# Performance work log

Hardware: AMD Instinct MI355X
Metric: run time of the kernel (lower is better)

Reference implementation:

```python
import jax, jax.numpy as jnp
import numpy as np

T, B = 1024, 128
IDIM, CDIM, N, M = 256, 512, 128, 64


def setup_inputs() -> dict:
    key = jax.random.key(0)
    ks = jax.random.split(key, 10)
    stdev = 5.0 / np.sqrt(IDIM + M + CDIM)  # matches _reset_controller
    u = lambda k, shp: jax.random.uniform(k, shp, jnp.float32, -stdev, stdev)
    return {
        "embs": jax.random.normal(ks[0], (T, B, IDIM), jnp.float32),
        "ilen": T // 2,
        # LSTM controller params (PyTorch layout: [4*cdim, in] / [4*cdim, cdim])
        "w_ih": u(ks[1], (4 * CDIM, IDIM + M)),
        "w_hh": u(ks[2], (4 * CDIM, CDIM)),
        "b_ih": jnp.zeros((4 * CDIM,), jnp.float32),
        "b_hh": jnp.zeros((4 * CDIM,), jnp.float32),
        "h0": jax.random.normal(ks[3], (CDIM,), jnp.float32) * 0.05,
        "c0": jax.random.normal(ks[4], (CDIM,), jnp.float32) * 0.05,
        "r0": jax.random.normal(ks[5], (1, M), jnp.float32) * 0.02,
        # memory head params (concrete subclass): write address / write value / read address
        "W_wa": jax.random.normal(ks[6], (N, CDIM), jnp.float32) * 0.02,
        "b_wa": jnp.zeros((N,), jnp.float32),
        "W_wv": jax.random.normal(ks[7], (M, IDIM), jnp.float32) * 0.02,
        "b_wv": jnp.zeros((M,), jnp.float32),
        "W_ra": jax.random.normal(ks[8], (N, CDIM), jnp.float32) * 0.02,
        "b_ra": jnp.zeros((N,), jnp.float32),
    }


def _forward(embs, w_ih, w_hh, b_ih, b_hh, h0, c0, r0,
             W_wa, b_wa, W_wv, b_wv, W_ra, b_ra, ilen):
    bsz = embs.shape[1]
    h = jnp.broadcast_to(h0, (bsz, CDIM))
    c = jnp.broadcast_to(c0, (bsz, CDIM))
    r = jnp.broadcast_to(r0, (bsz, M))
    mem = jnp.zeros((bsz, N, M), embs.dtype)
    b = b_ih + b_hh

    def step(carry, xt):
        h, c, r, mem = carry
        emb, t = xt  # emb: [B, idim]
        x = jnp.concatenate([emb, r], axis=-1)            # [B, idim+M]
        gates = x @ w_ih.T + h @ w_hh.T + b               # [B, 4*cdim]
        i, f, g, o = jnp.split(gates, 4, axis=-1)         # torch gate order i,f,g,o
        c_new = jax.nn.sigmoid(f) * c + jax.nn.sigmoid(i) * jnp.tanh(g)
        h_new = jax.nn.sigmoid(o) * jnp.tanh(c_new)       # controller_outp
        is_write = t < ilen
        # write(controller_outp, emb): additive write at softmax address
        wa = jax.nn.softmax(h_new @ W_wa.T + b_wa, axis=-1)   # [B, N]
        v = emb @ W_wv.T + b_wv                               # [B, M]
        mem_new = jnp.where(is_write, mem + wa[:, :, None] * v[:, None, :], mem)
        # read(controller_outp): softmax-addressed weighted sum over slots
        ra = jax.nn.softmax(h_new @ W_ra.T + b_ra, axis=-1)   # [B, N]
        r_read = jnp.einsum('bn,bnm->bm', ra, mem_new)        # [B, M]
        r_new = jnp.where(is_write, r, r_read)
        out = jnp.concatenate([h_new, r_new], axis=-1)        # [B, cdim+M]
        return (h_new, c_new, r_new, mem_new), out

    _, os = jax.lax.scan(step, (h, c, r, mem),
                         (embs, jnp.arange(embs.shape[0])))
    return os  # [T, B, cdim+M]


def reference(embs, ilen, w_ih, w_hh, b_ih, b_hh, h0, c0, r0,
              W_wa, b_wa, W_wv, b_wv, W_ra, b_ra):
    return _forward(embs, w_ih, w_hh, b_ih, b_hh, h0, c0, r0,
                    W_wa, b_wa, W_wv, b_wv, W_ra, b_ra, ilen)
```

## Files before the change

### kernel.cpp

```cpp
#include <hip/hip_runtime.h>

typedef _Float16 f16;
typedef __attribute__((ext_vector_type(8))) _Float16 half8;
typedef __attribute__((ext_vector_type(2))) _Float16 half2v;
typedef __attribute__((ext_vector_type(4))) float f32x4;
typedef __attribute__((ext_vector_type(4))) unsigned int u32x4;
typedef unsigned long long u64;

#define TSTEPS 1024

static const size_t OFF_WP   = 0;
static const size_t OFF_WVP  = 3407872;
static const size_t OFF_BIAS = 3440640;
static const size_t OFF_EMBP = 3448832;
static const size_t OFF_V    = 70557696;
static const size_t OFF_XH   = 87334912;
static const size_t OFF_XR   = 87597056;
static const size_t OFF_FLG  = 87629824;
static const size_t OFF_MEM  = 87630848;
static const size_t WS_NEED  = 91825152;


__global__ void marnn_packw(const float* __restrict__ w_ih, const float* __restrict__ w_hh,
                            const float* __restrict__ b_ih, const float* __restrict__ b_hh,
                            f16* __restrict__ WP, float* __restrict__ biasP) {
  int idx = blockIdx.x * 256 + threadIdx.x;
  if (idx < 2048) {
    int j = idx >> 2, g = idx & 3, rg = g * 512 + j;
    biasP[idx] = b_ih[rg] + b_hh[rg];
  }
  if (idx >= 1703936) return;
  int e = idx & 7, l = (idx >> 3) & 63;
  int q = idx >> 9;
  int ks = q % 26; int ntile = q / 26;
  int n = ntile * 16 + (l & 15);
  int k = ks * 32 + (l >> 4) * 8 + e;
  int j2 = n >> 2, g2 = n & 3, rg2 = g2 * 512 + j2;
  float v = (k < 320) ? w_ih[(size_t)rg2 * 320 + k] : w_hh[(size_t)rg2 * 512 + (k - 320)];
  WP[idx] = (f16)v;
}

__global__ void marnn_packwv(const float* __restrict__ W_wv, f16* __restrict__ WVP) {
  int idx = blockIdx.x * 256 + threadIdx.x;
  if (idx >= 16384) return;
  int e = idx & 7, l = (idx >> 3) & 63, ks = (idx >> 9) & 7, nt = idx >> 12;
  int n = nt * 16 + (l & 15);
  int k = ks * 32 + (l >> 4) * 8 + e;
  WVP[idx] = (f16)W_wv[n * 256 + k];
}

__global__ void marnn_packemb(const float* __restrict__ embs, f16* __restrict__ embsP) {
  const long total8 = (long)1024 * 128 * 32;
  const long stride = (long)gridDim.x * blockDim.x;
  for (long i8 = (long)blockIdx.x * blockDim.x + threadIdx.x; i8 < total8; i8 += stride) {
    int bl = (int)(i8 & 15), kc = (int)((i8 >> 4) & 31), bg = (int)((i8 >> 9) & 7);
    long t = i8 >> 12;
    const float* s = embs + ((t * 128) + bg * 16 + bl) * 256 + kc * 8;
    f32x4 a = *(const f32x4*)s, b = *(const f32x4*)(s + 4);
    half8 h;
    h[0]=(f16)a[0]; h[1]=(f16)a[1]; h[2]=(f16)a[2]; h[3]=(f16)a[3];
    h[4]=(f16)b[0]; h[5]=(f16)b[1]; h[6]=(f16)b[2]; h[7]=(f16)b[3];
    *(half8*)(embsP + i8 * 8) = h;
  }
}

__global__ __launch_bounds__(256)
void marnn_vpre(const f16* __restrict__ embsP, const f16* __restrict__ WVP,
                const float* __restrict__ b_wv, f16* __restrict__ Vh) {
  const int tb = blockIdx.x;
  const int wv = threadIdx.x >> 6, l = threadIdx.x & 63;
  half8 bf[8];
  #pragma unroll
  for (int ks = 0; ks < 8; ++ks)
    bf[ks] = *(const half8*)(WVP + ((size_t)(wv * 8 + ks) * 64 + l) * 8);
  const f16* ab = embsP + (size_t)tb * 4096;
  f32x4 acc = {0.f, 0.f, 0.f, 0.f};
  #pragma unroll
  for (int ks = 0; ks < 8; ++ks) {
    half8 af = *(const half8*)(ab + ((size_t)(ks * 4 + (l >> 4)) * 16 + (l & 15)) * 8);
    acc = __builtin_amdgcn_mfma_f32_16x16x32_f16(bf[ks], af, acc, 0, 0, 0);
  }
  const int b = (tb & 7) * 16 + (l & 15);
  const long t = tb >> 3;
  #pragma unroll
  for (int r = 0; r < 4; ++r) {
    int m = wv * 16 + (l >> 4) * 4 + r;
    Vh[((t * 128) + b) * 64 + m] = (f16)(acc[r] + b_wv[m]);
  }
}


struct __align__(16) MarnnSMem {
  f16  whead[128 * 512];
  char xl[26624];
  char un[4096];
};

__device__ __forceinline__ float marnn_dot8(half8 a, half8 b, float acc) {
#if __has_builtin(__builtin_amdgcn_fdot2)
  half2v a0 = {a[0],a[1]}, a1 = {a[2],a[3]}, a2 = {a[4],a[5]}, a3 = {a[6],a[7]};
  half2v b0 = {b[0],b[1]}, b1 = {b[2],b[3]}, b2 = {b[4],b[5]}, b3 = {b[6],b[7]};
  acc = __builtin_amdgcn_fdot2(a0, b0, acc, false);
  acc = __builtin_amdgcn_fdot2(a1, b1, acc, false);
  acc = __builtin_amdgcn_fdot2(a2, b2, acc, false);
  acc = __builtin_amdgcn_fdot2(a3, b3, acc, false);
#else
  #pragma unroll
  for (int e = 0; e < 8; ++e) acc += (float)a[e] * (float)b[e];
#endif
  return acc;
}

__device__ __forceinline__ float fast_sigmoid(float x) {
  return __builtin_amdgcn_rcpf(1.f + __expf(-x));
}
__device__ __forceinline__ float fast_tanh(float x) {
  return 1.f - 2.f * __builtin_amdgcn_rcpf(1.f + __expf(2.f * x));
}

__device__ __forceinline__ unsigned ld_flag(const unsigned* p) {
  return __hip_atomic_load(p, __ATOMIC_RELAXED, __HIP_MEMORY_SCOPE_AGENT);
}
__device__ __forceinline__ void st_flag(unsigned* p, unsigned v) {
  __hip_atomic_store(p, v, __ATOMIC_RELAXED, __HIP_MEMORY_SCOPE_AGENT);
}
__device__ __forceinline__ u64 ld_llc64(const void* p) {
  return __hip_atomic_load((const u64*)p, __ATOMIC_RELAXED, __HIP_MEMORY_SCOPE_AGENT);
}
__device__ __forceinline__ void st_llc32(void* p, unsigned v) {
  __hip_atomic_store((unsigned*)p, v, __ATOMIC_RELAXED, __HIP_MEMORY_SCOPE_AGENT);
}

__device__ __forceinline__ void poll16(const unsigned* line, unsigned ep) {
  int l = threadIdx.x & 63;
  for (;;) {
    unsigned v = (l < 16) ? ld_flag(line + l) : ep;
    if (__all((int)(v >= ep))) break;
    __builtin_amdgcn_s_sleep(1);
  }
  asm volatile("" ::: "memory");
}

__global__ __launch_bounds__(512, 1)
void marnn_main(const int* __restrict__ ilen_p, const float* __restrict__ h0,
                const float* __restrict__ c0, const float* __restrict__ r0,
                const float* __restrict__ W_wa, const float* __restrict__ b_wa,
                const float* __restrict__ W_ra, const float* __restrict__ b_ra,
                float* __restrict__ out, char* __restrict__ ws) {
  __shared__ MarnnSMem sm;

  const f16*   WP    = (const f16*)(ws + OFF_WP);
  const float* biasP = (const float*)(ws + OFF_BIAS);
  const f16*   embsP = (const f16*)(ws + OFF_EMBP);
  const f16*   Vh    = (const f16*)(ws + OFF_V);
  unsigned*    XH    = (unsigned*)(ws + OFF_XH);
  unsigned*    XR    = (unsigned*)(ws + OFF_XR);
  unsigned*    FLG   = (unsigned*)(ws + OFF_FLG);
  float*       MEMB  = (float*)(ws + OFF_MEM);

  const int blk = blockIdx.x, tid = threadIdx.x;
  const int wav = tid >> 6, lane = tid & 63;
  const int g = blk & 7, ns = blk >> 3;
  const int ilen = ilen_p[0];
  unsigned* gfh = FLG + g * 32;
  unsigned* gfr = gfh + 16;

  half8 bfr[26];
  {
    const f16* wpb = WP + ((size_t)(ns * 8 + wav) * 26) * 512 + lane * 8;
    #pragma unroll
    for (int ks = 0; ks < 26; ++ks) bfr[ks] = *(const half8*)(wpb + ks * 512);
  }

  auto loadWhead = [&](const float* Wsrc) {
    for (int i = tid; i < 8192; i += 512) {
      int n = i >> 6, slot = i & 63;
      const float* s = Wsrc + n * 512 + slot * 8;
      f32x4 a = *(const f32x4*)(s), b2 = *(const f32x4*)(s + 4);
      half8 hv;
      hv[0]=(f16)a[0]; hv[1]=(f16)a[1]; hv[2]=(f16)a[2]; hv[3]=(f16)a[3];
      hv[4]=(f16)b2[0]; hv[5]=(f16)b2[1]; hv[6]=(f16)b2[2]; hv[7]=(f16)b2[3];
      *(half8*)((char*)sm.whead + (n << 10) + (((slot + n) & 63) << 4)) = hv;
    }
  };
  loadWhead(ilen > 0 ? W_wa : W_ra);

  {
    const u32x4* s0 = (const u32x4*)(embsP + (size_t)g * 4096);
    ((u32x4*)sm.xl)[tid] = s0[tid];
    const float* hsrc0 = h0 + (tid >> 3) * 8;
    half8 hv;
    #pragma unroll
    for (int e = 0; e < 8; ++e) hv[e] = (f16)hsrc0[e];
    *(half8*)(sm.xl + 10240 + tid * 32) = hv;
    *(half8*)(sm.xl + 10240 + tid * 32 + 16) = hv;
  }
  __syncthreads();

  const int b_lane = lane & 15, sel = lane >> 4;
  const int jg = ns * 32 + wav * 4 + sel;
  float c = c0[jg];
  const f32x4 bias4 = *(const f32x4*)(biasP + jg * 4);
  const float r0v = (tid < 64) ? r0[tid] : 0.f;
  const int b = g * 16 + ns;

  const float bw0 = b_wa[lane], bw1 = b_wa[lane + 64];
  const float br0 = b_ra[lane], br1 = b_ra[lane + 64];
  const int gn = (wav & 3) * 32 + (lane & 31);
  const int kq = ((wav >> 2) << 1) | (lane >> 5);

  half8 rf0, rf1;
  #pragma unroll
  for (int e = 0; e < 8; ++e) {
    rf0[e] = (f16)r0[sel * 8 + e];
    rf1[e] = (f16)r0[32 + sel * 8 + e];
  }

  for (int t = 0; t < TSTEPS; ++t) {
    const int par = t & 1, nxt = par ^ 1;
    const bool iswrite = (t < ilen);

    u32x4 sa = {0u, 0u, 0u, 0u};
    if (t + 1 < TSTEPS)
      sa = ((const u32x4*)(embsP + (((size_t)(t + 1) * 8) + g) * 4096))[tid];
    half8 vh = {};
    if (iswrite && wav == 4 && lane < 8)
      vh = *(const half8*)(Vh + ((size_t)t * 128 + b) * 64 + lane * 8);

    if (t > ilen && wav == 0) {
      poll16(gfr, (unsigned)(t - ilen));
      const u64* rsrc = (const u64*)XR + ((size_t)par * 8 + g) * 256;
      #pragma unroll
      for (int i = 0; i < 4; ++i) {
        int v = i * 64 + lane;
        u64 d = ld_llc64(rsrc + v);
        int bb = v >> 4;
        int m0 = (v & 15) * 4;
        char* dst = sm.xl + 8192 + ((m0 >= 32) ? 1024 : 0)
                    + (((m0 & 31) >> 3) * 256) + bb * 16 + (m0 & 7) * 2;
        *(u64*)dst = d;
      }
    }
    f32x4 acc0 = {0.f, 0.f, 0.f, 0.f}, acc1 = {0.f, 0.f, 0.f, 0.f};
    const char* xb = sm.xl + sel * 256 + b_lane * 16;
    #pragma unroll
    for (int ks = 0; ks < 8; ++ks) {
      half8 af = *(const half8*)(xb + ks * 1024);
      if (ks & 1) acc1 = __builtin_amdgcn_mfma_f32_16x16x32_f16(bfr[ks], af, acc1, 0, 0, 0);
      else        acc0 = __builtin_amdgcn_mfma_f32_16x16x32_f16(bfr[ks], af, acc0, 0, 0, 0);
    }
    #pragma unroll
    for (int ks = 10; ks < 26; ++ks) {
      half8 af = *(const half8*)(xb + ks * 1024);
      if (ks & 1) acc1 = __builtin_amdgcn_mfma_f32_16x16x32_f16(bfr[ks], af, acc1, 0, 0, 0);
      else        acc0 = __builtin_amdgcn_mfma_f32_16x16x32_f16(bfr[ks], af, acc0, 0, 0, 0);
    }
    if (t <= ilen) {
      acc0 = __builtin_amdgcn_mfma_f32_16x16x32_f16(bfr[8], rf0, acc0, 0, 0, 0);
      acc1 = __builtin_amdgcn_mfma_f32_16x16x32_f16(bfr[9], rf1, acc1, 0, 0, 0);
    } else {
      __syncthreads();
      acc0 = __builtin_amdgcn_mfma_f32_16x16x32_f16(bfr[8], *(const half8*)(xb + 8 * 1024), acc0, 0, 0, 0);
      acc1 = __builtin_amdgcn_mfma_f32_16x16x32_f16(bfr[9], *(const half8*)(xb + 9 * 1024), acc1, 0, 0, 0);
    }
    const f32x4 acc = acc0 + acc1;

    float h;
    {
      float si = fast_sigmoid(acc[0] + bias4[0]);
      float sf = fast_sigmoid(acc[1] + bias4[1]);
      float so = fast_sigmoid(acc[3] + bias4[3]);
      c = sf * c + si * fast_tanh(acc[2] + bias4[2]);
      h = so * fast_tanh(c);
      union { f16 f; unsigned short u; } cv; cv.f = (f16)h;
      unsigned hu = cv.u;
      unsigned pu = __shfl_down(hu, 16, 64);
      if (!(sel & 1))
        st_llc32(XH + ((size_t)nxt * 8 + g) * 4096
                   + ns * 256 + wav * 32 + b_lane * 2 + (sel >> 1),
                 hu | (pu << 16));
    }
    asm volatile("s_waitcnt vmcnt(0)" ::: "memory");
    __syncthreads();
    if (tid == 0) st_flag(gfh + ns, (unsigned)(t + 1));
    __builtin_nontemporal_store(h, &out[(size_t)t * 73728 + (g * 16 + b_lane) * 576 + jg]);
    if (wav == 0) poll16(gfh, (unsigned)(t + 1));
    __syncthreads();

    {
      ((u32x4*)sm.xl)[tid] = sa;
      const u64* hsrc = (const u64*)XH + ((size_t)nxt * 8 + g) * 2048;
      #pragma unroll
      for (int i = 0; i < 4; ++i) {
        int v = i * 512 + tid;
        u64 d = ld_llc64(hsrc + v);
        int nsp = v >> 7;
        int wvp = (v >> 4) & 7;
        int bb = v & 15;
        int j0 = nsp * 32 + wvp * 4;
        char* dst = sm.xl + 10240 + ((j0 >> 3) * 256) + bb * 16 + (j0 & 7) * 2;
        *(u64*)dst = d;
      }
    }
    __syncthreads();

    if (t == ilen) { loadWhead(W_ra); __syncthreads(); }
    float* vpart = (float*)sm.un;
    float* vred  = (float*)(sm.un + 1024);
    float* vsec  = (float*)(sm.un + 3072);
    {
      if (iswrite && wav == 4 && lane < 8) {
        f32x4 lo = {(float)vh[0], (float)vh[1], (float)vh[2], (float)vh[3]};
        f32x4 hi = {(float)vh[4], (float)vh[5], (float)vh[6], (float)vh[7]};
        *(f32x4*)(vsec + lane * 8) = lo;
        *(f32x4*)(vsec + lane * 8 + 4) = hi;
      }
      const char* wrow = (const char*)sm.whead + (gn << 10);
      const char* hbase = sm.xl + 10240 + ns * 16;
      float av0 = 0.f, av1 = 0.f;
      #pragma unroll
      for (int i = 0; i < 16; i += 2) {
        int s0 = kq * 16 + i;
        av0 = marnn_dot8(*(const half8*)(wrow + (((s0 + gn) & 63) << 4)),
                         *(const half8*)(hbase + s0 * 256), av0);
        av1 = marnn_dot8(*(const half8*)(wrow + (((s0 + 1 + gn) & 63) << 4)),
                         *(const half8*)(hbase + (s0 + 1) * 256), av1);
      }
      float av = av0 + av1;
      av += __shfl_xor(av, 32, 64);
      if (lane < 32) vpart[((wav >> 2) << 7) + gn] = av;
    }
    __syncthreads();

    float p0, p1;
    {
      float l0 = vpart[lane] + vpart[128 + lane] + (iswrite ? bw0 : br0);
      float l1 = vpart[64 + lane] + vpart[192 + lane] + (iswrite ? bw1 : br1);
      float mx = fmaxf(l0, l1);
      #pragma unroll
      for (int off = 32; off > 0; off >>= 1) mx = fmaxf(mx, __shfl_xor(mx, off, 64));
      float e0 = __expf(l0 - mx), e1 = __expf(l1 - mx);
      float s = e0 + e1;
      #pragma unroll
      for (int off = 32; off > 0; off >>= 1) s += __shfl_xor(s, off, 64);
      float inv = __builtin_amdgcn_rcpf(s);
      p0 = e0 * inv; p1 = e1 * inv;
    }

    if (iswrite) {
      int n = tid >> 2;
      float pA = __shfl(p0, n & 63, 64);
      float pB = __shfl(p1, n & 63, 64);
      float p = (n < 64) ? pA : pB;
      float* mrow = MEMB + (((size_t)b) * 128 + n) * 64 + (tid & 3) * 16;
      const float* vv = vsec + (tid & 3) * 16;
      #pragma unroll
      for (int i2 = 0; i2 < 16; i2 += 4) {
        f32x4 mm = *(f32x4*)(mrow + i2);
        f32x4 v4 = *(const f32x4*)(vv + i2);
        mm = mm + p * v4;
        *(f32x4*)(mrow + i2) = mm;
      }
      if (tid < 64)
        __builtin_nontemporal_store(r0v, &out[(size_t)t * 73728 + b * 576 + 512 + tid]);
    } else {
      const int m = tid & 63;
      const float* mcol = MEMB + (((size_t)b) * 128 + wav * 16) * 64 + m;
      float a0 = 0.f, a1 = 0.f;
      #pragma unroll
      for (int n2 = 0; n2 < 16; n2 += 2) {
        float q0 = __shfl((wav < 4) ? p0 : p1, (wav * 16 + n2) & 63, 64);
        float q1 = __shfl((wav < 4) ? p0 : p1, (wav * 16 + n2 + 1) & 63, 64);
        a0 = fmaf(q0, mcol[n2 * 64], a0);
        a1 = fmaf(q1, mcol[(n2 + 1) * 64], a1);
      }
      vred[wav * 64 + m] = a0 + a1;
      __syncthreads();
      if (tid < 64) {
        float rv = 0.f;
        #pragma unroll
        for (int nc = 0; nc < 8; ++nc) rv += vred[nc * 64 + tid];
        union { f16 f; unsigned short u; } cr; cr.f = (f16)rv;
        unsigned ru = cr.u;
        unsigned rp = __shfl_down(ru, 1, 64);
        if (!(tid & 1))
          st_llc32(XR + ((size_t)nxt * 8 + g) * 512 + ns * 32 + (tid >> 1),
                   ru | (rp << 16));
        asm volatile("s_waitcnt vmcnt(0)" ::: "memory");
        if (tid == 0) st_flag(gfr + ns, (unsigned)(t - ilen + 1));
        __builtin_nontemporal_store(rv, &out[(size_t)t * 73728 + b * 576 + 512 + tid]);
      }
    }
  }
}


extern "C" void kernel_launch(void* const* d_in, const int* in_sizes, int n_in,
                              void* d_out, int out_size, void* d_ws, size_t ws_size,
                              hipStream_t stream) {
  const float* embs = (const float*)d_in[0];
  const int*   ilen = (const int*)d_in[1];
  const float* w_ih = (const float*)d_in[2];
  const float* w_hh = (const float*)d_in[3];
  const float* b_ih = (const float*)d_in[4];
  const float* b_hh = (const float*)d_in[5];
  const float* h0   = (const float*)d_in[6];
  const float* c0   = (const float*)d_in[7];
  const float* r0   = (const float*)d_in[8];
  const float* W_wa = (const float*)d_in[9];
  const float* b_wa = (const float*)d_in[10];
  const float* W_wv = (const float*)d_in[11];
  const float* b_wv = (const float*)d_in[12];
  const float* W_ra = (const float*)d_in[13];
  const float* b_ra = (const float*)d_in[14];
  float* out = (float*)d_out;
  char* ws = (char*)d_ws;
  if (ws_size < WS_NEED) return;

  hipMemsetAsync(ws + OFF_FLG, 0, 1024, stream);
  hipMemsetAsync(ws + OFF_MEM, 0, 4194304, stream);
  marnn_packw<<<6656, 256, 0, stream>>>(w_ih, w_hh, b_ih, b_hh,
                                        (f16*)(ws + OFF_WP), (float*)(ws + OFF_BIAS));
  marnn_packwv<<<64, 256, 0, stream>>>(W_wv, (f16*)(ws + OFF_WVP));
  marnn_packemb<<<2048, 256, 0, stream>>>(embs, (f16*)(ws + OFF_EMBP));
  marnn_vpre<<<8192, 256, 0, stream>>>((const f16*)(ws + OFF_EMBP), (const f16*)(ws + OFF_WVP),
                                       b_wv, (f16*)(ws + OFF_V));
  marnn_main<<<128, 512, 0, stream>>>(ilen, h0, c0, r0, W_wa, b_wa, W_ra, b_ra, out, ws);
}
```

Measured before the change: 6.163 ms.

## Distribute head-address projection across blocks via MFMA partial sums exchanged in L2

Each block no longer keeps the full 128x512 head weight in LDS and computes all address logits with dot products. Instead, each block computes a partial logit for its own 32-column slice of h with one MFMA from register-resident fragments. The partials are published through a global exchange buffer with an extra flag, and each block sums the 16 partials before the softmax. This removes the per-step full head matvec and the weight reload at the write/read switch. In exchange it adds two more block barriers and an extra cross-block exchange in fp16, which may cost precision. The fetch of the read vector is also moved inside the read-phase branch.

New measurement: 6.196 ms. No clear change (+0.5%).

```diff
diff --git a/kernel.cpp b/kernel.cpp
--- a/kernel.cpp
+++ b/kernel.cpp
@@ -2,7 +2,6 @@
 
 typedef _Float16 f16;
 typedef __attribute__((ext_vector_type(8))) _Float16 half8;
-typedef __attribute__((ext_vector_type(2))) _Float16 half2v;
 typedef __attribute__((ext_vector_type(4))) float f32x4;
 typedef __attribute__((ext_vector_type(4))) unsigned int u32x4;
 typedef unsigned long long u64;
@@ -16,9 +15,10 @@
 static const size_t OFF_V    = 70557696;
 static const size_t OFF_XH   = 87334912;
 static const size_t OFF_XR   = 87597056;
-static const size_t OFF_FLG  = 87629824;
-static const size_t OFF_MEM  = 87630848;
-static const size_t WS_NEED  = 91825152;
+static const size_t OFF_XP   = 87629824;
+static const size_t OFF_FLG  = 88678400;
+static const size_t OFF_MEM  = 88680448;
+static const size_t WS_NEED  = 92874752;
 
 
 __global__ void marnn_packw(const float* __restrict__ w_ih, const float* __restrict__ w_hh,
@@ -91,25 +91,13 @@
 
 
 struct __align__(16) MarnnSMem {
-  f16  whead[128 * 512];
-  char xl[26624];
-  char un[4096];
+  char  xl[26624];
+  f16   hlocal[512];
+  f16   plocal[2048];
+  float pacc[1024];
+  float vred[512];
+  float vsec[64];
 };
-
-__device__ __forceinline__ float marnn_dot8(half8 a, half8 b, float acc) {
-#if __has_builtin(__builtin_amdgcn_fdot2)
-  half2v a0 = {a[0],a[1]}, a1 = {a[2],a[3]}, a2 = {a[4],a[5]}, a3 = {a[6],a[7]};
-  half2v b0 = {b[0],b[1]}, b1 = {b[2],b[3]}, b2 = {b[4],b[5]}, b3 = {b[6],b[7]};
-  acc = __builtin_amdgcn_fdot2(a0, b0, acc, false);
-  acc = __builtin_amdgcn_fdot2(a1, b1, acc, false);
-  acc = __builtin_amdgcn_fdot2(a2, b2, acc, false);
-  acc = __builtin_amdgcn_fdot2(a3, b3, acc, false);
-#else
-  #pragma unroll
-  for (int e = 0; e < 8; ++e) acc += (float)a[e] * (float)b[e];
-#endif
-  return acc;
-}
 
 __device__ __forceinline__ float fast_sigmoid(float x) {
   return __builtin_amdgcn_rcpf(1.f + __expf(-x));
@@ -129,12 +117,26 @@
 }
 __device__ __forceinline__ void st_llc32(void* p, unsigned v) {
   __hip_atomic_store((unsigned*)p, v, __ATOMIC_RELAXED, __HIP_MEMORY_SCOPE_AGENT);
+}
+__device__ __forceinline__ void st_llc64(void* p, u64 v) {
+  __hip_atomic_store((u64*)p, v, __ATOMIC_RELAXED, __HIP_MEMORY_SCOPE_AGENT);
 }
 
 __device__ __forceinline__ void poll16(const unsigned* line, unsigned ep) {
   int l = threadIdx.x & 63;
   for (;;) {
     unsigned v = (l < 16) ? ld_flag(line + l) : ep;
+    if (__all((int)(v >= ep))) break;
+    __builtin_amdgcn_s_sleep(1);
+  }
+  asm volatile("" ::: "memory");
+}
+__device__ __forceinline__ void poll2x16(const unsigned* ha, const unsigned* pa, unsigned ep) {
+  int l = threadIdx.x & 63;
+  for (;;) {
+    unsigned v = ep;
+    if (l < 16) v = ld_flag(ha + l);
+    else if (l < 32) v = ld_flag(pa + (l - 16));
     if (__all((int)(v >= ep))) break;
     __builtin_amdgcn_s_sleep(1);
   }
@@ -155,6 +157,7 @@
   const f16*   Vh    = (const f16*)(ws + OFF_V);
   unsigned*    XH    = (unsigned*)(ws + OFF_XH);
   unsigned*    XR    = (unsigned*)(ws + OFF_XR);
+  u64*         XP    = (u64*)(ws + OFF_XP);
   unsigned*    FLG   = (unsigned*)(ws + OFF_FLG);
   float*       MEMB  = (float*)(ws + OFF_MEM);
 
@@ -162,8 +165,9 @@
   const int wav = tid >> 6, lane = tid & 63;
   const int g = blk & 7, ns = blk >> 3;
   const int ilen = ilen_p[0];
-  unsigned* gfh = FLG + g * 32;
+  unsigned* gfh = FLG + g * 64;
   unsigned* gfr = gfh + 16;
+  unsigned* gfp = gfh + 32;
 
   half8 bfr[26];
   {
@@ -171,19 +175,16 @@
     #pragma unroll
     for (int ks = 0; ks < 26; ++ks) bfr[ks] = *(const half8*)(wpb + ks * 512);
   }
-
-  auto loadWhead = [&](const float* Wsrc) {
-    for (int i = tid; i < 8192; i += 512) {
-      int n = i >> 6, slot = i & 63;
-      const float* s = Wsrc + n * 512 + slot * 8;
-      f32x4 a = *(const f32x4*)(s), b2 = *(const f32x4*)(s + 4);
-      half8 hv;
-      hv[0]=(f16)a[0]; hv[1]=(f16)a[1]; hv[2]=(f16)a[2]; hv[3]=(f16)a[3];
-      hv[4]=(f16)b2[0]; hv[5]=(f16)b2[1]; hv[6]=(f16)b2[2]; hv[7]=(f16)b2[3];
-      *(half8*)((char*)sm.whead + (n << 10) + (((slot + n) & 63) << 4)) = hv;
-    }
-  };
-  loadWhead(ilen > 0 ? W_wa : W_ra);
+  half8 wafrag, rafrag;
+  {
+    const int nrow = wav * 16 + (lane & 15);
+    const int jcol = ns * 32 + ((lane >> 4) << 3);
+    #pragma unroll
+    for (int e = 0; e < 8; ++e) {
+      wafrag[e] = (f16)W_wa[nrow * 512 + jcol + e];
+      rafrag[e] = (f16)W_ra[nrow * 512 + jcol + e];
+    }
+  }
 
   {
     const u32x4* s0 = (const u32x4*)(embsP + (size_t)g * 4096);
@@ -206,8 +207,6 @@
 
   const float bw0 = b_wa[lane], bw1 = b_wa[lane + 64];
   const float br0 = b_ra[lane], br1 = b_ra[lane + 64];
-  const int gn = (wav & 3) * 32 + (lane & 31);
-  const int kq = ((wav >> 2) << 1) | (lane >> 5);
 
   half8 rf0, rf1;
   #pragma unroll
@@ -227,20 +226,6 @@
     if (iswrite && wav == 4 && lane < 8)
       vh = *(const half8*)(Vh + ((size_t)t * 128 + b) * 64 + lane * 8);
 
-    if (t > ilen && wav == 0) {
-      poll16(gfr, (unsigned)(t - ilen));
-      const u64* rsrc = (const u64*)XR + ((size_t)par * 8 + g) * 256;
-      #pragma unroll
-      for (int i = 0; i < 4; ++i) {
-        int v = i * 64 + lane;
-        u64 d = ld_llc64(rsrc + v);
-        int bb = v >> 4;
-        int m0 = (v & 15) * 4;
-        char* dst = sm.xl + 8192 + ((m0 >= 32) ? 1024 : 0)
-                    + (((m0 & 31) >> 3) * 256) + bb * 16 + (m0 & 7) * 2;
-        *(u64*)dst = d;
-      }
-    }
     f32x4 acc0 = {0.f, 0.f, 0.f, 0.f}, acc1 = {0.f, 0.f, 0.f, 0.f};
     const char* xb = sm.xl + sel * 256 + b_lane * 16;
     #pragma unroll
@@ -259,6 +244,20 @@
       acc0 = __builtin_amdgcn_mfma_f32_16x16x32_f16(bfr[8], rf0, acc0, 0, 0, 0);
       acc1 = __builtin_amdgcn_mfma_f32_16x16x32_f16(bfr[9], rf1, acc1, 0, 0, 0);
     } else {
+      if (wav == 0) {
+        poll16(gfr, (unsigned)(t - ilen));
+        const u64* rsrc = (const u64*)XR + ((size_t)par * 8 + g) * 256;
+        #pragma unroll
+        for (int i = 0; i < 4; ++i) {
+          int v = i * 64 + lane;
+          u64 d = ld_llc64(rsrc + v);
+          int bb = v >> 4;
+          int m0 = (v & 15) * 4;
+          char* dst = sm.xl + 8192 + ((m0 >= 32) ? 1024 : 0)
+                      + (((m0 & 31) >> 3) * 256) + bb * 16 + (m0 & 7) * 2;
+          *(u64*)dst = d;
+        }
+      }
       __syncthreads();
       acc0 = __builtin_amdgcn_mfma_f32_16x16x32_f16(bfr[8], *(const half8*)(xb + 8 * 1024), acc0, 0, 0, 0);
       acc1 = __builtin_amdgcn_mfma_f32_16x16x32_f16(bfr[9], *(const half8*)(xb + 9 * 1024), acc1, 0, 0, 0);
@@ -272,6 +271,7 @@
       float so = fast_sigmoid(acc[3] + bias4[3]);
       c = sf * c + si * fast_tanh(acc[2] + bias4[2]);
       h = so * fast_tanh(c);
+      sm.hlocal[b_lane * 32 + wav * 4 + sel] = (f16)h;
       union { f16 f; unsigned short u; } cv; cv.f = (f16)h;
       unsigned hu = cv.u;
       unsigned pu = __shfl_down(hu, 16, 64);
@@ -280,11 +280,29 @@
                    + ns * 256 + wav * 32 + b_lane * 2 + (sel >> 1),
                  hu | (pu << 16));
     }
+    __syncthreads();
+
+    {
+      half8 bfh = *(const half8*)(sm.hlocal + b_lane * 32 + sel * 8);
+      f32x4 pp = {0.f, 0.f, 0.f, 0.f};
+      pp = __builtin_amdgcn_mfma_f32_16x16x32_f16(iswrite ? wafrag : rafrag, bfh, pp, 0, 0, 0);
+      #pragma unroll
+      for (int r = 0; r < 4; ++r)
+        sm.plocal[b_lane * 128 + wav * 16 + sel * 4 + r] = (f16)pp[r];
+    }
+    __syncthreads();
+    {
+      u64 pw = *(const u64*)(sm.plocal + tid * 4);
+      st_llc64(XP + (((size_t)nxt * 8 + g) * 16 + ns) * 512 + tid, pw);
+    }
     asm volatile("s_waitcnt vmcnt(0)" ::: "memory");
     __syncthreads();
-    if (tid == 0) st_flag(gfh + ns, (unsigned)(t + 1));
+    if (tid == 0) {
+      st_flag(gfh + ns, (unsigned)(t + 1));
+      st_flag(gfp + ns, (unsigned)(t + 1));
+    }
     __builtin_nontemporal_store(h, &out[(size_t)t * 73728 + (g * 16 + b_lane) * 576 + jg]);
-    if (wav == 0) poll16(gfh, (unsigned)(t + 1));
+    if (wav == 0) poll2x16(gfh, gfp, (unsigned)(t + 1));
     __syncthreads();
 
     {
@@ -294,48 +312,40 @@
       for (int i = 0; i < 4; ++i) {
         int v = i * 512 + tid;
         u64 d = ld_llc64(hsrc + v);
-        int nsp = v >> 7;
-        int wvp = (v >> 4) & 7;
-        int bb = v & 15;
+        int nsp = v >> 7, wvp = (v >> 4) & 7, bb = v & 15;
         int j0 = nsp * 32 + wvp * 4;
         char* dst = sm.xl + 10240 + ((j0 >> 3) * 256) + bb * 16 + (j0 & 7) * 2;
         *(u64*)dst = d;
       }
-    }
-    __syncthreads();
-
-    if (t == ilen) { loadWhead(W_ra); __syncthreads(); }
-    float* vpart = (float*)sm.un;
-    float* vred  = (float*)(sm.un + 1024);
-    float* vsec  = (float*)(sm.un + 3072);
-    {
+      u64 d2 = ld_llc64(XP + (((size_t)nxt * 8 + g) * 16 + (tid >> 5)) * 512
+                           + ns * 32 + (tid & 31));
+      union { u64 u; f16 hh[4]; } pu2; pu2.u = d2;
+      float q0 = (float)pu2.hh[0], q1 = (float)pu2.hh[1];
+      float q2 = (float)pu2.hh[2], q3 = (float)pu2.hh[3];
+      q0 += __shfl_xor(q0, 32, 64); q1 += __shfl_xor(q1, 32, 64);
+      q2 += __shfl_xor(q2, 32, 64); q3 += __shfl_xor(q3, 32, 64);
+      if (lane < 32) {
+        f32x4 qq = {q0, q1, q2, q3};
+        *(f32x4*)(sm.pacc + wav * 128 + lane * 4) = qq;
+      }
       if (iswrite && wav == 4 && lane < 8) {
         f32x4 lo = {(float)vh[0], (float)vh[1], (float)vh[2], (float)vh[3]};
         f32x4 hi = {(float)vh[4], (float)vh[5], (float)vh[6], (float)vh[7]};
-        *(f32x4*)(vsec + lane * 8) = lo;
-        *(f32x4*)(vsec + lane * 8 + 4) = hi;
-      }
-      const char* wrow = (const char*)sm.whead + (gn << 10);
-      const char* hbase = sm.xl + 10240 + ns * 16;
-      float av0 = 0.f, av1 = 0.f;
-      #pragma unroll
-      for (int i = 0; i < 16; i += 2) {
-        int s0 = kq * 16 + i;
-        av0 = marnn_dot8(*(const half8*)(wrow + (((s0 + gn) & 63) << 4)),
-                         *(const half8*)(hbase + s0 * 256), av0);
-        av1 = marnn_dot8(*(const half8*)(wrow + (((s0 + 1 + gn) & 63) << 4)),
-                         *(const half8*)(hbase + (s0 + 1) * 256), av1);
-      }
-      float av = av0 + av1;
-      av += __shfl_xor(av, 32, 64);
-      if (lane < 32) vpart[((wav >> 2) << 7) + gn] = av;
+        *(f32x4*)(sm.vsec + lane * 8) = lo;
+        *(f32x4*)(sm.vsec + lane * 8 + 4) = hi;
+      }
     }
     __syncthreads();
 
     float p0, p1;
     {
-      float l0 = vpart[lane] + vpart[128 + lane] + (iswrite ? bw0 : br0);
-      float l1 = vpart[64 + lane] + vpart[192 + lane] + (iswrite ? bw1 : br1);
+      float l0 = iswrite ? bw0 : br0;
+      float l1 = iswrite ? bw1 : br1;
+      #pragma unroll
+      for (int w = 0; w < 8; ++w) {
+        l0 += sm.pacc[w * 128 + lane];
+        l1 += sm.pacc[w * 128 + 64 + lane];
+      }
       float mx = fmaxf(l0, l1);
       #pragma unroll
       for (int off = 32; off > 0; off >>= 1) mx = fmaxf(mx, __shfl_xor(mx, off, 64));
@@ -353,7 +363,7 @@
       float pB = __shfl(p1, n & 63, 64);
       float p = (n < 64) ? pA : pB;
       float* mrow = MEMB + (((size_t)b) * 128 + n) * 64 + (tid & 3) * 16;
-      const float* vv = vsec + (tid & 3) * 16;
+      const float* vv = sm.vsec + (tid & 3) * 16;
       #pragma unroll
       for (int i2 = 0; i2 < 16; i2 += 4) {
         f32x4 mm = *(f32x4*)(mrow + i2);
@@ -374,12 +384,12 @@
         a0 = fmaf(q0, mcol[n2 * 64], a0);
         a1 = fmaf(q1, mcol[(n2 + 1) * 64], a1);
       }
-      vred[wav * 64 + m] = a0 + a1;
+      sm.vred[wav * 64 + m] = a0 + a1;
       __syncthreads();
       if (tid < 64) {
         float rv = 0.f;
         #pragma unroll
-        for (int nc = 0; nc < 8; ++nc) rv += vred[nc * 64 + tid];
+        for (int nc = 0; nc < 8; ++nc) rv += sm.vred[nc * 64 + tid];
         union { f16 f; unsigned short u; } cr; cr.f = (f16)rv;
         unsigned ru = cr.u;
         unsigned rp = __shfl_down(ru, 1, 64);
@@ -417,7 +427,7 @@
   char* ws = (char*)d_ws;
   if (ws_size < WS_NEED) return;
 
-  hipMemsetAsync(ws + OFF_FLG, 0, 1024, stream);
+  hipMemsetAsync(ws + OFF_FLG, 0, 2048, stream);
   hipMemsetAsync(ws + OFF_MEM, 0, 4194304, stream);
   marnn_packw<<<6656, 256, 0, stream>>>(w_ih, w_hh, b_ih, b_hh,
                                         (f16*)(ws + OFF_WP), (float*)(ws + OFF_BIAS));
```
